# Kernel tuning notes

Measured on AMD Instinct MI355X. Metric: run time of the kernel, lower is better.

Reference implementation:

```python
import jax, jax.numpy as jnp
import numpy as np

DIM = 1024
B, S = 4, 2048

def setup_inputs() -> dict:
    key = jax.random.key(0)
    ks = jax.random.split(key, 4)
    x = jax.random.normal(ks[0], (B, S, DIM), dtype=jnp.float32)
    mask = jax.random.randint(ks[1], (B, S, S), 0, 2, dtype=jnp.int32)
    Wqkv = jax.random.normal(ks[2], (DIM, 3 * DIM), dtype=jnp.float32) / np.sqrt(DIM)
    bqkv = jnp.zeros((3 * DIM,), dtype=jnp.float32)
    Wout = jax.random.normal(ks[3], (DIM, DIM), dtype=jnp.float32) / np.sqrt(DIM)
    bout = jnp.zeros((DIM,), dtype=jnp.float32)
    return {"x": x, "mask": mask, "Wqkv": Wqkv, "bqkv": bqkv, "Wout": Wout, "bout": bout}

def reference(x, mask, Wqkv, bqkv, Wout, bout):
    dim = x.shape[-1]
    qkv = x @ Wqkv + bqkv                      # [B,S,3*dim]
    q, k, v = jnp.split(qkv, 3, axis=-1)       # each [B,S,dim]
    scores = jnp.einsum('bqd,bkd->bqk', q, k) / jnp.sqrt(jnp.float32(dim))
    # faithful to torch: masked positions set to 1e-10 (NOT -inf)
    scores = jnp.where(mask == 0, jnp.float32(1e-10), scores)
    attn = jax.nn.softmax(scores, axis=-1)     # dropout is identity in eval
    out = jnp.einsum('bqk,bkd->bqd', attn, v)  # [B,S,dim]
    return out @ Wout + bout
```

## Files before the change

kernel.cpp:

```cpp
#include <hip/hip_runtime.h>


typedef __attribute__((ext_vector_type(8))) short short8;
typedef __attribute__((ext_vector_type(4))) float f32x4;
typedef unsigned short u16;

#define SEQ 2048
#define NB 4

static __device__ __forceinline__ u16 f2bf(float f) {
    unsigned int u = __builtin_bit_cast(unsigned int, f);
    u += 0x7fffu + ((u >> 16) & 1u);
    return (u16)(u >> 16);
}
static __device__ __forceinline__ float bf2f(u16 h) {
    unsigned int u = ((unsigned int)h) << 16;
    return __builtin_bit_cast(float, u);
}

static __device__ __forceinline__ void gld16(const u16* l, const u16* g) {
    __builtin_amdgcn_global_load_lds(
        (__attribute__((address_space(1))) void*)(g),
        (__attribute__((address_space(3))) void*)(l),
        16, 0, 0);
}

__global__ __launch_bounds__(256) void cvt_bf16(const float* __restrict__ s,
                                                u16* __restrict__ d, long n) {
    long i = ((long)blockIdx.x * 256 + threadIdx.x) * 8;
    if (i >= n) return;
    f32x4 a = *(const f32x4*)(s + i);
    f32x4 b = *(const f32x4*)(s + i + 4);
    short8 o;
    o[0] = (short)f2bf(a.x); o[1] = (short)f2bf(a.y);
    o[2] = (short)f2bf(a.z); o[3] = (short)f2bf(a.w);
    o[4] = (short)f2bf(b.x); o[5] = (short)f2bf(b.y);
    o[6] = (short)f2bf(b.z); o[7] = (short)f2bf(b.w);
    *(short8*)(d + i) = o;
}

__global__ __launch_bounds__(256) void transpose_cvt(const float* __restrict__ in,
                                                     u16* __restrict__ out,
                                                     int R, int C) {
    __shared__ float t[32][33];
    const int c0 = blockIdx.x * 32;
    const int r0 = blockIdx.y * 32;
    const int x = threadIdx.x & 31;
    const int y = (threadIdx.x >> 5) * 4;
    #pragma unroll
    for (int i = 0; i < 4; i++)
        t[y + i][x] = in[(long)(r0 + y + i) * C + c0 + x];
    __syncthreads();
    #pragma unroll
    for (int i = 0; i < 4; i++)
        out[(long)(c0 + y + i) * R + r0 + x] = f2bf(t[x][y + i]);
}

__global__ __launch_bounds__(256) void transpose_v(const u16* __restrict__ qkv,
                                                   u16* __restrict__ vt) {
    __shared__ u16 t[32][33];
    const int b = blockIdx.z;
    const int s0 = blockIdx.y * 32;
    const int d0 = blockIdx.x * 32;
    const int x = threadIdx.x & 31;
    const int y = (threadIdx.x >> 5) * 4;
    const u16* src = qkv + (long)b * SEQ * 3072 + 2048;
    u16* dst = vt + (long)b * 1024 * SEQ;
    #pragma unroll
    for (int i = 0; i < 4; i++)
        t[y + i][x] = src[(long)(s0 + y + i) * 3072 + d0 + x];
    __syncthreads();
    #pragma unroll
    for (int i = 0; i < 4; i++)
        dst[(long)(d0 + y + i) * SEQ + s0 + x] = t[x][y + i];
}

template<int EPI>
__global__ __launch_bounds__(512) void gemm256(
    const u16* __restrict__ Ap, long lda, long aBatch,
    const u16* __restrict__ Bp, long ldb, long bBatch,
    void* __restrict__ Cp, long ldc, long cBatch,
    const float* __restrict__ bias, float scale, int K, int nbx)
{
    __shared__ __attribute__((aligned(16))) u16 lds[2][4][8192];

    const int T = K >> 6;
    const int tid = threadIdx.x;
    const int lane = tid & 63;
    const int wave = tid >> 6;
    const int wm = wave >> 2;
    const int wn = wave & 3;
    const int m16 = lane & 15;
    const int quad = lane >> 4;
    const int b = blockIdx.z;

    const int nwg = gridDim.x;
    int wg = blockIdx.x;
    if ((nwg & 7) == 0)
        wg = (wg & 7) * (nwg >> 3) + (wg >> 3);
    const int bx = wg % nbx;
    const int by = wg / nbx;
    const long gm0 = (long)by * 256;
    const long gn0 = (long)bx * 256;

    const u16* A = Ap + (long)b * aBatch;
    const u16* B = Bp + (long)b * bBatch;

    const int rl = lane >> 3;
    const int lsl = ((lane & 7) ^ rl) * 8;
    const long aR = gm0 + wave * 8 + rl;
    const long bR = gn0 + (wave >> 2) * 64 + (wave & 3) * 8 + rl;

#define STG_A(h, tt) do { \
    const int tc_ = ((tt) < T) ? (tt) : (tt) - 2; \
    const long kc_ = (long)(tc_ << 6); \
    const int sl_ = tc_ & 1; \
    gld16(&lds[sl_][h][wave * 512],       A + (aR + (h) * 64) * lda + kc_ + lsl); \
    gld16(&lds[sl_][h][(8 + wave) * 512], A + (aR + 128 + (h) * 64) * lda + kc_ + lsl); \
} while (0)
#define STG_B(h, tt) do { \
    const int tc_ = ((tt) < T) ? (tt) : (tt) - 2; \
    const long kc_ = (long)(tc_ << 6); \
    const int sl_ = tc_ & 1; \
    gld16(&lds[sl_][2 + (h)][wave * 512],       B + (bR + (h) * 32) * ldb + kc_ + lsl); \
    gld16(&lds[sl_][2 + (h)][(8 + wave) * 512], B + (bR + 128 + (h) * 32) * ldb + kc_ + lsl); \
} while (0)

    const int s0 = quad ^ (m16 & 7);
    const int aBase = (wm * 64 + m16) * 64;
    const int bBase = (wn * 32 + m16) * 64;
    const int aoff0 = aBase + s0 * 8, aoff1 = aBase + (s0 ^ 4) * 8;
    const int boff0 = bBase + s0 * 8, boff1 = bBase + (s0 ^ 4) * 8;

    short8 aF[4][2], b0F[2][2], b1F[2][2];
    f32x4 acc[8][4];
    #pragma unroll
    for (int mi = 0; mi < 8; mi++)
        #pragma unroll
        for (int ni = 0; ni < 4; ni++)
            acc[mi][ni] = (f32x4){0.f, 0.f, 0.f, 0.f};

#define LD_A(sl, h) do { \
    const u16* p_ = &lds[sl][h][0]; \
    _Pragma("unroll") \
    for (int mfl_ = 0; mfl_ < 4; ++mfl_) { \
        aF[mfl_][0] = *(const short8*)(p_ + aoff0 + mfl_ * 1024); \
        aF[mfl_][1] = *(const short8*)(p_ + aoff1 + mfl_ * 1024); \
    } \
} while (0)
#define LD_B(sl, h, BF) do { \
    const u16* p_ = &lds[sl][2 + (h)][0]; \
    _Pragma("unroll") \
    for (int nj_ = 0; nj_ < 2; ++nj_) { \
        BF[nj_][0] = *(const short8*)(p_ + boff0 + nj_ * 1024); \
        BF[nj_][1] = *(const short8*)(p_ + boff1 + nj_ * 1024); \
    } \
} while (0)
#define MFMAQ(mh, nh, BF) do { \
    _Pragma("unroll") \
    for (int mi_ = 0; mi_ < 4; ++mi_) \
    _Pragma("unroll") \
    for (int nj_ = 0; nj_ < 2; ++nj_) { \
        acc[(mh)*4+mi_][(nh)*2+nj_] = __builtin_amdgcn_mfma_f32_16x16x32_bf16( \
            aF[mi_][0], BF[nj_][0], acc[(mh)*4+mi_][(nh)*2+nj_], 0, 0, 0); \
        acc[(mh)*4+mi_][(nh)*2+nj_] = __builtin_amdgcn_mfma_f32_16x16x32_bf16( \
            aF[mi_][1], BF[nj_][1], acc[(mh)*4+mi_][(nh)*2+nj_], 0, 0, 0); \
    } \
} while (0)
#define BAR() asm volatile("s_barrier" ::: "memory")
#define VM8() asm volatile("s_waitcnt vmcnt(8)" ::: "memory")
#define SETP(p) __builtin_amdgcn_s_setprio(p)

    STG_A(0, 0); STG_B(0, 0); STG_B(1, 0); STG_A(1, 0);
    STG_A(0, 1); STG_B(0, 1); STG_B(1, 1); STG_A(1, 1);
    VM8();
    BAR();
    LD_B(0, 0, b0F);

    for (int t = 0; t < T; ++t) {
        const int buf = t & 1, nb = buf ^ 1;
        LD_A(buf, 0);
        SETP(1); MFMAQ(0, 0, b0F); SETP(0);
        BAR();
        LD_B(buf, 1, b1F);
        STG_A(0, t + 2);
        STG_B(0, t + 2);
        SETP(1); MFMAQ(0, 1, b1F); SETP(0);
        BAR();
        LD_A(buf, 1);
        STG_B(1, t + 2);
        SETP(1); MFMAQ(1, 0, b0F); SETP(0);
        BAR();
        STG_A(1, t + 2);
        VM8();
        BAR();
        LD_B(nb, 0, b0F);
        SETP(1); MFMAQ(1, 1, b1F); SETP(0);
    }

    const long row0 = gm0 + wm * 128 + quad * 4;
    if (EPI == 0 || EPI == 1) {
        u16* C = (u16*)Cp + (long)b * cBatch;
        #pragma unroll
        for (int ni = 0; ni < 4; ++ni) {
            const long col = gn0 + wn * 64 + (ni >> 1) * 32 + (ni & 1) * 16 + m16;
            const float bv = (EPI == 0 && bias) ? bias[col] : 0.f;
            #pragma unroll
            for (int mi = 0; mi < 8; ++mi) {
                const long rb = row0 + (mi >> 2) * 64 + (mi & 3) * 16;
                #pragma unroll
                for (int r = 0; r < 4; ++r) {
                    const float vv = (EPI == 1) ? acc[mi][ni][r] * scale
                                                : acc[mi][ni][r] + bv;
                    C[(rb + r) * ldc + col] = f2bf(vv);
                }
            }
        }
    } else {
        float* C = (float*)Cp + (long)b * cBatch;
        #pragma unroll
        for (int ni = 0; ni < 4; ++ni) {
            const long col = gn0 + wn * 64 + (ni >> 1) * 32 + (ni & 1) * 16 + m16;
            const float bv = bias ? bias[col] : 0.f;
            #pragma unroll
            for (int mi = 0; mi < 8; ++mi) {
                const long rb = row0 + (mi >> 2) * 64 + (mi & 3) * 16;
                #pragma unroll
                for (int r = 0; r < 4; ++r)
                    C[(rb + r) * ldc + col] = acc[mi][ni][r] + bv;
            }
        }
    }
#undef STG_A
#undef STG_B
#undef LD_A
#undef LD_B
#undef MFMAQ
#undef BAR
#undef VM8
#undef SETP
}

template<int EPI>
__global__ __launch_bounds__(256) void gemm128(
    const u16* __restrict__ Ap, long lda, long aBatch,
    const u16* __restrict__ Bp, long ldb, long bBatch,
    void* __restrict__ Cp, long ldc, long cBatch,
    const float* __restrict__ bias,
    float scale, int K)
{
    __shared__ __attribute__((aligned(16))) u16 As[128 * 64];
    __shared__ __attribute__((aligned(16))) u16 Bs[128 * 64];

    const int tid = threadIdx.x;
    const int lane = tid & 63;
    const int wave = tid >> 6;
    const int b = blockIdx.z;
    const long m0 = (long)blockIdx.y * 128;
    const long n0 = (long)blockIdx.x * 128;

    const u16* A = Ap + (long)b * aBatch;
    const u16* B = Bp + (long)b * bBatch;

    const int wm = (wave >> 1) * 64;
    const int wn = (wave & 1) * 64;
    const int m16 = lane & 15;
    const int quad = lane >> 4;

    const int srow = lane >> 3;
    const int skk = (lane & 7) * 8;

    f32x4 acc[4][4];
    #pragma unroll
    for (int mi = 0; mi < 4; mi++)
        #pragma unroll
        for (int ni = 0; ni < 4; ni++)
            acc[mi][ni] = (f32x4){0.f, 0.f, 0.f, 0.f};

    for (int k0 = 0; k0 < K; k0 += 64) {
        #pragma unroll
        for (int c = 0; c < 4; c++) {
            const int r = wave * 32 + c * 8 + srow;
            gld16(As + (wave * 4 + c) * 512, A + (m0 + r) * lda + k0 + skk);
            gld16(Bs + (wave * 4 + c) * 512, B + (n0 + r) * ldb + k0 + skk);
        }
        __syncthreads();

        #pragma unroll
        for (int ks = 0; ks < 2; ks++) {
            short8 af[4], bf[4];
            #pragma unroll
            for (int i = 0; i < 4; i++) {
                af[i] = *(const short8*)&As[(wm + i * 16 + m16) * 64 + ks * 32 + quad * 8];
                bf[i] = *(const short8*)&Bs[(wn + i * 16 + m16) * 64 + ks * 32 + quad * 8];
            }
            #pragma unroll
            for (int mi = 0; mi < 4; mi++)
                #pragma unroll
                for (int ni = 0; ni < 4; ni++)
                    acc[mi][ni] = __builtin_amdgcn_mfma_f32_16x16x32_bf16(
                        af[mi], bf[ni], acc[mi][ni], 0, 0, 0);
        }
        __syncthreads();
    }

    const long row_base = m0 + wm + quad * 4;
    if (EPI == 0) {
        u16* C = (u16*)Cp + (long)b * cBatch;
        #pragma unroll
        for (int ni = 0; ni < 4; ni++) {
            const long col = n0 + wn + ni * 16 + m16;
            const float bv = bias ? bias[col] : 0.f;
            #pragma unroll
            for (int mi = 0; mi < 4; mi++)
                #pragma unroll
                for (int r = 0; r < 4; r++)
                    C[(row_base + mi * 16 + r) * ldc + col] = f2bf(acc[mi][ni][r] + bv);
        }
    } else if (EPI == 1) {
        u16* C = (u16*)Cp + (long)b * cBatch;
        #pragma unroll
        for (int ni = 0; ni < 4; ni++) {
            const long col = n0 + wn + ni * 16 + m16;
            #pragma unroll
            for (int mi = 0; mi < 4; mi++)
                #pragma unroll
                for (int r = 0; r < 4; r++)
                    C[(row_base + mi * 16 + r) * ldc + col] = f2bf(acc[mi][ni][r] * scale);
        }
    } else {
        float* C = (float*)Cp + (long)b * cBatch;
        #pragma unroll
        for (int ni = 0; ni < 4; ni++) {
            const long col = n0 + wn + ni * 16 + m16;
            const float bv = bias ? bias[col] : 0.f;
            #pragma unroll
            for (int mi = 0; mi < 4; mi++)
                #pragma unroll
                for (int r = 0; r < 4; r++)
                    C[(row_base + mi * 16 + r) * ldc + col] = acc[mi][ni][r] + bv;
        }
    }
}

__global__ __launch_bounds__(256) void softmax2048(u16* __restrict__ S,
                                                   const int* __restrict__ mask) {
    const long row = blockIdx.x;
    u16* p = S + row * SEQ;
    const int* mrow = mask + row * SEQ;
    const int tid = threadIdx.x;

    short8 v = *(const short8*)(p + tid * 8);
    uint4 mw0 = *(const uint4*)(mrow + tid * 8);
    uint4 mw1 = *(const uint4*)(mrow + tid * 8 + 4);
    const unsigned int* mwv = (const unsigned int*)&mw0;

    float f[8];
    #pragma unroll
    for (int j = 0; j < 8; j++) {
        const unsigned int mv = (j < 4) ? mwv[j] : ((const unsigned int*)&mw1)[j - 4];
        f[j] = (mv == 0u) ? 1e-10f : bf2f((u16)v[j]);
    }

    float m = f[0];
    #pragma unroll
    for (int j = 1; j < 8; j++) m = fmaxf(m, f[j]);
    #pragma unroll
    for (int i = 1; i < 64; i <<= 1) m = fmaxf(m, __shfl_xor(m, i));

    __shared__ float redm[4], reds[4];
    if ((tid & 63) == 0) redm[tid >> 6] = m;
    __syncthreads();
    m = fmaxf(fmaxf(redm[0], redm[1]), fmaxf(redm[2], redm[3]));

    float e[8], s = 0.f;
    #pragma unroll
    for (int j = 0; j < 8; j++) { e[j] = __expf(f[j] - m); s += e[j]; }
    #pragma unroll
    for (int i = 1; i < 64; i <<= 1) s += __shfl_xor(s, i);
    if ((tid & 63) == 0) reds[tid >> 6] = s;
    __syncthreads();
    s = reds[0] + reds[1] + reds[2] + reds[3];

    const float inv = 1.f / s;
    short8 o;
    #pragma unroll
    for (int j = 0; j < 8; j++) o[j] = (short)f2bf(e[j] * inv);
    *(short8*)(p + tid * 8) = o;
}

extern "C" void kernel_launch(void* const* d_in, const int* in_sizes, int n_in,
                              void* d_out, int out_size, void* d_ws, size_t ws_size,
                              hipStream_t stream) {
    const float* x    = (const float*)d_in[0];
    const int*   mask = (const int*)d_in[1];
    const float* Wqkv = (const float*)d_in[2];
    const float* bqkv = (const float*)d_in[3];
    const float* Wout = (const float*)d_in[4];
    const float* bout = (const float*)d_in[5];
    float* out = (float*)d_out;

    char* ws = (char*)d_ws;
    u16* xh   = (u16*)(ws + 0);
    u16* wqt  = (u16*)(ws + 16777216);
    u16* sc   = (u16*)(ws + 0);
    u16* wot  = (u16*)(ws + 33554432);
    u16* qkv  = (u16*)(ws + 35651584);
    u16* attn = (u16*)(ws + 35651584);
    u16* vt   = (u16*)(ws + 85983232);

    cvt_bf16<<<4096, 256, 0, stream>>>(x, xh, 8388608);
    transpose_cvt<<<dim3(96, 32), 256, 0, stream>>>(Wqkv, wqt, 1024, 3072);
    transpose_cvt<<<dim3(32, 32), 256, 0, stream>>>(Wout, wot, 1024, 1024);

    gemm256<0><<<dim3(384, 1, 1), 512, 0, stream>>>(
        xh, 1024, 0, wqt, 1024, 0, qkv, 3072, 0, bqkv, 1.f, 1024, 12);

    transpose_v<<<dim3(32, 64, NB), 256, 0, stream>>>(qkv, vt);

    gemm256<1><<<dim3(64, 1, NB), 512, 0, stream>>>(
        qkv, 3072, (long)SEQ * 3072, qkv + 1024, 3072, (long)SEQ * 3072,
        sc, SEQ, (long)SEQ * SEQ, nullptr, 0.03125f, 1024, 8);

    softmax2048<<<dim3(NB * SEQ), 256, 0, stream>>>(sc, mask);

    gemm128<0><<<dim3(8, 16, NB), 256, 0, stream>>>(
        sc, SEQ, (long)SEQ * SEQ, vt, SEQ, (long)1024 * SEQ,
        attn, 1024, (long)SEQ * 1024, nullptr, 1.f, 2048);

    gemm128<2><<<dim3(8, 64, 1), 256, 0, stream>>>(
        attn, 1024, 0, wot, 1024, 0, out, 1024, 0, bout, 1.f, 1024);
}
```

Measured before the change: 236.0 us.

## Restructure 8-wave GEMM main loop into barrier-fenced MFMA phases with shifted staging

Reorders the software pipeline of the 256x256 GEMM main loop: each MFMA quarter is now wrapped in barriers, an LDS wait, and scheduling barriers. Global-to-LDS staging of one B half is delayed by one iteration, with vmcnt thresholds adjusted to match. The aim is a ping-pong style schedule where memory and MFMA phases alternate cleanly and the compiler cannot interleave them. It adds extra barriers per iteration and carries a risk of stalls or hazards if the shifted staging order and wait counts are off.

```diff
diff --git a/kernel.cpp b/kernel.cpp
--- a/kernel.cpp
+++ b/kernel.cpp
@@ -169,33 +169,39 @@
 } while (0)
 #define BAR() asm volatile("s_barrier" ::: "memory")
 #define VM8() asm volatile("s_waitcnt vmcnt(8)" ::: "memory")
+#define VM10() asm volatile("s_waitcnt vmcnt(10)" ::: "memory")
+#define LGKM8() asm volatile("s_waitcnt lgkmcnt(8)" ::: "memory")
+#define LGKM0() asm volatile("s_waitcnt lgkmcnt(0)" ::: "memory")
+#define SGB0() __builtin_amdgcn_sched_barrier(0)
 #define SETP(p) __builtin_amdgcn_s_setprio(p)
-
-    STG_A(0, 0); STG_B(0, 0); STG_B(1, 0); STG_A(1, 0);
-    STG_A(0, 1); STG_B(0, 1); STG_B(1, 1); STG_A(1, 1);
-    VM8();
+#define PHASE_MFMA(mh, nh, BF) do { \
+    BAR(); LGKM0(); SGB0(); \
+    SETP(1); MFMAQ(mh, nh, BF); SETP(0); \
+    SGB0(); BAR(); \
+} while (0)
+
+    STG_A(0, 0); STG_B(0, 0); STG_A(1, 0); STG_B(1, 0);
+    STG_A(0, 1); STG_B(0, 1); STG_A(1, 1);
+    VM10();
     BAR();
-    LD_B(0, 0, b0F);
 
     for (int t = 0; t < T; ++t) {
-        const int buf = t & 1, nb = buf ^ 1;
+        const int buf = t & 1;
         LD_A(buf, 0);
-        SETP(1); MFMAQ(0, 0, b0F); SETP(0);
-        BAR();
+        LD_B(buf, 0, b0F);
+        STG_B(1, t + 1);
+        LGKM8();
+        VM8();
+        PHASE_MFMA(0, 0, b0F);
         LD_B(buf, 1, b1F);
         STG_A(0, t + 2);
+        PHASE_MFMA(0, 1, b1F);
+        LD_A(buf, 1);
         STG_B(0, t + 2);
-        SETP(1); MFMAQ(0, 1, b1F); SETP(0);
-        BAR();
-        LD_A(buf, 1);
-        STG_B(1, t + 2);
-        SETP(1); MFMAQ(1, 0, b0F); SETP(0);
-        BAR();
+        PHASE_MFMA(1, 0, b0F);
         STG_A(1, t + 2);
-        VM8();
-        BAR();
-        LD_B(nb, 0, b0F);
-        SETP(1); MFMAQ(1, 1, b1F); SETP(0);
+        VM10();
+        PHASE_MFMA(1, 1, b1F);
     }
 
     const long row0 = gm0 + wm * 128 + quad * 4;
@@ -238,7 +244,12 @@
 #undef MFMAQ
 #undef BAR
 #undef VM8
+#undef VM10
+#undef LGKM8
+#undef LGKM0
+#undef SGB0
 #undef SETP
+#undef PHASE_MFMA
 }
 
 template<int EPI>
```

Measured after the change: 238.2 us. No clear change (+0.9%).

## Replace interleaved gemm256 pipeline with simple double-buffered tile loop

Applied to the files above, without the earlier changes.

Replaces the four-phase interleaved stage/compute schedule in the 256x256 GEMM with a plain double-buffer scheme. Each tile's loads are issued into the other LDS buffer, then all A/B fragments are computed, with a full __syncthreads between tiles. This drops the fine-grained barriers, the vmcnt waits and the MFMA priority hints. It also reorders the epilogue loops in both GEMM kernels so each thread writes along a row, with bias values hoisted. It risks less overlap between load and compute and higher register pressure, since all B fragments are held at once.

```diff
diff --git a/kernel.cpp b/kernel.cpp
--- a/kernel.cpp
+++ b/kernel.cpp
@@ -76,7 +76,7 @@
 }
 
 template<int EPI>
-__global__ __launch_bounds__(512) void gemm256(
+__global__ __launch_bounds__(512) void gemm256d(
     const u16* __restrict__ Ap, long lda, long aBatch,
     const u16* __restrict__ Bp, long ldb, long bBatch,
     void* __restrict__ Cp, long ldc, long cBatch,
@@ -111,19 +111,17 @@
     const long aR = gm0 + wave * 8 + rl;
     const long bR = gn0 + (wave >> 2) * 64 + (wave & 3) * 8 + rl;
 
-#define STG_A(h, tt) do { \
-    const int tc_ = ((tt) < T) ? (tt) : (tt) - 2; \
-    const long kc_ = (long)(tc_ << 6); \
-    const int sl_ = tc_ & 1; \
-    gld16(&lds[sl_][h][wave * 512],       A + (aR + (h) * 64) * lda + kc_ + lsl); \
-    gld16(&lds[sl_][h][(8 + wave) * 512], A + (aR + 128 + (h) * 64) * lda + kc_ + lsl); \
-} while (0)
-#define STG_B(h, tt) do { \
-    const int tc_ = ((tt) < T) ? (tt) : (tt) - 2; \
-    const long kc_ = (long)(tc_ << 6); \
-    const int sl_ = tc_ & 1; \
-    gld16(&lds[sl_][2 + (h)][wave * 512],       B + (bR + (h) * 32) * ldb + kc_ + lsl); \
-    gld16(&lds[sl_][2 + (h)][(8 + wave) * 512], B + (bR + 128 + (h) * 32) * ldb + kc_ + lsl); \
+#define STGD(sl, tt) do { \
+    const long kc_ = (long)(tt) << 6; \
+    u16* l_ = &lds[sl][0][0]; \
+    gld16(l_ + 0 * 8192 + wave * 512,       A + (aR)       * lda + kc_ + lsl); \
+    gld16(l_ + 0 * 8192 + (8 + wave) * 512, A + (aR + 128) * lda + kc_ + lsl); \
+    gld16(l_ + 1 * 8192 + wave * 512,       A + (aR + 64)  * lda + kc_ + lsl); \
+    gld16(l_ + 1 * 8192 + (8 + wave) * 512, A + (aR + 192) * lda + kc_ + lsl); \
+    gld16(l_ + 2 * 8192 + wave * 512,       B + (bR)       * ldb + kc_ + lsl); \
+    gld16(l_ + 2 * 8192 + (8 + wave) * 512, B + (bR + 128) * ldb + kc_ + lsl); \
+    gld16(l_ + 3 * 8192 + wave * 512,       B + (bR + 32)  * ldb + kc_ + lsl); \
+    gld16(l_ + 3 * 8192 + (8 + wave) * 512, B + (bR + 160) * ldb + kc_ + lsl); \
 } while (0)
 
     const int s0 = quad ^ (m16 & 7);
@@ -140,105 +138,102 @@
         for (int ni = 0; ni < 4; ni++)
             acc[mi][ni] = (f32x4){0.f, 0.f, 0.f, 0.f};
 
-#define LD_A(sl, h) do { \
-    const u16* p_ = &lds[sl][h][0]; \
+#define TILE_COMPUTE(sl) do { \
+    const u16* l = &lds[sl][0][0]; \
     _Pragma("unroll") \
-    for (int mfl_ = 0; mfl_ < 4; ++mfl_) { \
-        aF[mfl_][0] = *(const short8*)(p_ + aoff0 + mfl_ * 1024); \
-        aF[mfl_][1] = *(const short8*)(p_ + aoff1 + mfl_ * 1024); \
+    for (int mfl = 0; mfl < 4; ++mfl) { \
+        aF[mfl][0] = *(const short8*)(l + aoff0 + mfl * 1024); \
+        aF[mfl][1] = *(const short8*)(l + aoff1 + mfl * 1024); \
     } \
+    _Pragma("unroll") \
+    for (int nj = 0; nj < 2; ++nj) { \
+        b0F[nj][0] = *(const short8*)(l + 2 * 8192 + boff0 + nj * 1024); \
+        b0F[nj][1] = *(const short8*)(l + 2 * 8192 + boff1 + nj * 1024); \
+        b1F[nj][0] = *(const short8*)(l + 3 * 8192 + boff0 + nj * 1024); \
+        b1F[nj][1] = *(const short8*)(l + 3 * 8192 + boff1 + nj * 1024); \
+    } \
+    _Pragma("unroll") \
+    for (int mi = 0; mi < 4; ++mi) \
+        _Pragma("unroll") \
+        for (int nj = 0; nj < 4; ++nj) { \
+            const short8* bf = (nj < 2) ? &b0F[nj][0] : &b1F[nj - 2][0]; \
+            acc[mi][nj] = __builtin_amdgcn_mfma_f32_16x16x32_bf16( \
+                aF[mi][0], bf[0], acc[mi][nj], 0, 0, 0); \
+            acc[mi][nj] = __builtin_amdgcn_mfma_f32_16x16x32_bf16( \
+                aF[mi][1], bf[1], acc[mi][nj], 0, 0, 0); \
+        } \
+    _Pragma("unroll") \
+    for (int mfl = 0; mfl < 4; ++mfl) { \
+        aF[mfl][0] = *(const short8*)(l + 1 * 8192 + aoff0 + mfl * 1024); \
+        aF[mfl][1] = *(const short8*)(l + 1 * 8192 + aoff1 + mfl * 1024); \
+    } \
+    _Pragma("unroll") \
+    for (int mi = 0; mi < 4; ++mi) \
+        _Pragma("unroll") \
+        for (int nj = 0; nj < 4; ++nj) { \
+            const short8* bf = (nj < 2) ? &b0F[nj][0] : &b1F[nj - 2][0]; \
+            acc[4 + mi][nj] = __builtin_amdgcn_mfma_f32_16x16x32_bf16( \
+                aF[mi][0], bf[0], acc[4 + mi][nj], 0, 0, 0); \
+            acc[4 + mi][nj] = __builtin_amdgcn_mfma_f32_16x16x32_bf16( \
+                aF[mi][1], bf[1], acc[4 + mi][nj], 0, 0, 0); \
+        } \
 } while (0)
-#define LD_B(sl, h, BF) do { \
-    const u16* p_ = &lds[sl][2 + (h)][0]; \
-    _Pragma("unroll") \
-    for (int nj_ = 0; nj_ < 2; ++nj_) { \
-        BF[nj_][0] = *(const short8*)(p_ + boff0 + nj_ * 1024); \
-        BF[nj_][1] = *(const short8*)(p_ + boff1 + nj_ * 1024); \
-    } \
-} while (0)
-#define MFMAQ(mh, nh, BF) do { \
-    _Pragma("unroll") \
-    for (int mi_ = 0; mi_ < 4; ++mi_) \
-    _Pragma("unroll") \
-    for (int nj_ = 0; nj_ < 2; ++nj_) { \
-        acc[(mh)*4+mi_][(nh)*2+nj_] = __builtin_amdgcn_mfma_f32_16x16x32_bf16( \
-            aF[mi_][0], BF[nj_][0], acc[(mh)*4+mi_][(nh)*2+nj_], 0, 0, 0); \
-        acc[(mh)*4+mi_][(nh)*2+nj_] = __builtin_amdgcn_mfma_f32_16x16x32_bf16( \
-            aF[mi_][1], BF[nj_][1], acc[(mh)*4+mi_][(nh)*2+nj_], 0, 0, 0); \
-    } \
-} while (0)
-#define BAR() asm volatile("s_barrier" ::: "memory")
-#define VM8() asm volatile("s_waitcnt vmcnt(8)" ::: "memory")
-#define SETP(p) __builtin_amdgcn_s_setprio(p)
-
-    STG_A(0, 0); STG_B(0, 0); STG_B(1, 0); STG_A(1, 0);
-    STG_A(0, 1); STG_B(0, 1); STG_B(1, 1); STG_A(1, 1);
-    VM8();
-    BAR();
-    LD_B(0, 0, b0F);
-
-    for (int t = 0; t < T; ++t) {
-        const int buf = t & 1, nb = buf ^ 1;
-        LD_A(buf, 0);
-        SETP(1); MFMAQ(0, 0, b0F); SETP(0);
-        BAR();
-        LD_B(buf, 1, b1F);
-        STG_A(0, t + 2);
-        STG_B(0, t + 2);
-        SETP(1); MFMAQ(0, 1, b1F); SETP(0);
-        BAR();
-        LD_A(buf, 1);
-        STG_B(1, t + 2);
-        SETP(1); MFMAQ(1, 0, b0F); SETP(0);
-        BAR();
-        STG_A(1, t + 2);
-        VM8();
-        BAR();
-        LD_B(nb, 0, b0F);
-        SETP(1); MFMAQ(1, 1, b1F); SETP(0);
+
+    STGD(0, 0);
+    __syncthreads();
+
+    for (int t = 0; t < T; t += 2) {
+        if (t + 1 < T) STGD(1, t + 1);
+        TILE_COMPUTE(0);
+        __syncthreads();
+        if (t + 2 < T) STGD(0, t + 2);
+        TILE_COMPUTE(1);
+        __syncthreads();
     }
 
     const long row0 = gm0 + wm * 128 + quad * 4;
+    const long colbase = gn0 + wn * 64 + m16;
     if (EPI == 0 || EPI == 1) {
         u16* C = (u16*)Cp + (long)b * cBatch;
-        #pragma unroll
-        for (int ni = 0; ni < 4; ++ni) {
-            const long col = gn0 + wn * 64 + (ni >> 1) * 32 + (ni & 1) * 16 + m16;
-            const float bv = (EPI == 0 && bias) ? bias[col] : 0.f;
-            #pragma unroll
-            for (int mi = 0; mi < 8; ++mi) {
-                const long rb = row0 + (mi >> 2) * 64 + (mi & 3) * 16;
-                #pragma unroll
-                for (int r = 0; r < 4; ++r) {
+        float bv[4];
+        #pragma unroll
+        for (int ni = 0; ni < 4; ++ni)
+            bv[ni] = (EPI == 0 && bias)
+                   ? bias[colbase + (ni >> 1) * 32 + (ni & 1) * 16] : 0.f;
+        #pragma unroll
+        for (int mi = 0; mi < 8; ++mi) {
+            const long rb = row0 + (mi >> 2) * 64 + (mi & 3) * 16;
+            #pragma unroll
+            for (int r = 0; r < 4; ++r) {
+                u16* Crow = C + (rb + r) * ldc + colbase;
+                #pragma unroll
+                for (int ni = 0; ni < 4; ++ni) {
                     const float vv = (EPI == 1) ? acc[mi][ni][r] * scale
-                                                : acc[mi][ni][r] + bv;
-                    C[(rb + r) * ldc + col] = f2bf(vv);
+                                                : acc[mi][ni][r] + bv[ni];
+                    Crow[(ni >> 1) * 32 + (ni & 1) * 16] = f2bf(vv);
                 }
             }
         }
     } else {
         float* C = (float*)Cp + (long)b * cBatch;
-        #pragma unroll
-        for (int ni = 0; ni < 4; ++ni) {
-            const long col = gn0 + wn * 64 + (ni >> 1) * 32 + (ni & 1) * 16 + m16;
-            const float bv = bias ? bias[col] : 0.f;
-            #pragma unroll
-            for (int mi = 0; mi < 8; ++mi) {
-                const long rb = row0 + (mi >> 2) * 64 + (mi & 3) * 16;
-                #pragma unroll
-                for (int r = 0; r < 4; ++r)
-                    C[(rb + r) * ldc + col] = acc[mi][ni][r] + bv;
+        float bv[4];
+        #pragma unroll
+        for (int ni = 0; ni < 4; ++ni)
+            bv[ni] = bias ? bias[colbase + (ni >> 1) * 32 + (ni & 1) * 16] : 0.f;
+        #pragma unroll
+        for (int mi = 0; mi < 8; ++mi) {
+            const long rb = row0 + (mi >> 2) * 64 + (mi & 3) * 16;
+            #pragma unroll
+            for (int r = 0; r < 4; ++r) {
+                float* Crow = C + (rb + r) * ldc + colbase;
+                #pragma unroll
+                for (int ni = 0; ni < 4; ++ni)
+                    Crow[(ni >> 1) * 32 + (ni & 1) * 16] = acc[mi][ni][r] + bv[ni];
             }
         }
     }
-#undef STG_A
-#undef STG_B
-#undef LD_A
-#undef LD_B
-#undef MFMAQ
-#undef BAR
-#undef VM8
-#undef SETP
+#undef STGD
+#undef TILE_COMPUTE
 }
 
 template<int EPI>
@@ -305,41 +300,48 @@
     }
 
     const long row_base = m0 + wm + quad * 4;
+    const long colbase = n0 + wn + m16;
     if (EPI == 0) {
         u16* C = (u16*)Cp + (long)b * cBatch;
-        #pragma unroll
-        for (int ni = 0; ni < 4; ni++) {
-            const long col = n0 + wn + ni * 16 + m16;
-            const float bv = bias ? bias[col] : 0.f;
-            #pragma unroll
-            for (int mi = 0; mi < 4; mi++)
-                #pragma unroll
-                for (int r = 0; r < 4; r++)
-                    C[(row_base + mi * 16 + r) * ldc + col] = f2bf(acc[mi][ni][r] + bv);
-        }
+        float bv[4];
+        #pragma unroll
+        for (int ni = 0; ni < 4; ni++)
+            bv[ni] = bias ? bias[colbase + ni * 16] : 0.f;
+        #pragma unroll
+        for (int mi = 0; mi < 4; mi++)
+            #pragma unroll
+            for (int r = 0; r < 4; r++) {
+                u16* Crow = C + (row_base + mi * 16 + r) * ldc + colbase;
+                #pragma unroll
+                for (int ni = 0; ni < 4; ni++)
+                    Crow[ni * 16] = f2bf(acc[mi][ni][r] + bv[ni]);
+            }
     } else if (EPI == 1) {
         u16* C = (u16*)Cp + (long)b * cBatch;
         #pragma unroll
-        for (int ni = 0; ni < 4; ni++) {
-            const long col = n0 + wn + ni * 16 + m16;
-            #pragma unroll
-            for (int mi = 0; mi < 4; mi++)
-                #pragma unroll
-                for (int r = 0; r < 4; r++)
-                    C[(row_base + mi * 16 + r) * ldc + col] = f2bf(acc[mi][ni][r] * scale);
-        }
+        for (int mi = 0; mi < 4; mi++)
+            #pragma unroll
+            for (int r = 0; r < 4; r++) {
+                u16* Crow = C + (row_base + mi * 16 + r) * ldc + colbase;
+                #pragma unroll
+                for (int ni = 0; ni < 4; ni++)
+                    Crow[ni * 16] = f2bf(acc[mi][ni][r] * scale);
+            }
     } else {
         float* C = (float*)Cp + (long)b * cBatch;
-        #pragma unroll
-        for (int ni = 0; ni < 4; ni++) {
-            const long col = n0 + wn + ni * 16 + m16;
-            const float bv = bias ? bias[col] : 0.f;
-            #pragma unroll
-            for (int mi = 0; mi < 4; mi++)
-                #pragma unroll
-                for (int r = 0; r < 4; r++)
-                    C[(row_base + mi * 16 + r) * ldc + col] = acc[mi][ni][r] + bv;
-        }
+        float bv[4];
+        #pragma unroll
+        for (int ni = 0; ni < 4; ni++)
+            bv[ni] = bias ? bias[colbase + ni * 16] : 0.f;
+        #pragma unroll
+        for (int mi = 0; mi < 4; mi++)
+            #pragma unroll
+            for (int r = 0; r < 4; r++) {
+                float* Crow = C + (row_base + mi * 16 + r) * ldc + colbase;
+                #pragma unroll
+                for (int ni = 0; ni < 4; ni++)
+                    Crow[ni * 16] = acc[mi][ni][r] + bv[ni];
+            }
     }
 }
 
@@ -413,12 +415,12 @@
     transpose_cvt<<<dim3(96, 32), 256, 0, stream>>>(Wqkv, wqt, 1024, 3072);
     transpose_cvt<<<dim3(32, 32), 256, 0, stream>>>(Wout, wot, 1024, 1024);
 
-    gemm256<0><<<dim3(384, 1, 1), 512, 0, stream>>>(
+    gemm256d<0><<<dim3(384, 1, 1), 512, 0, stream>>>(
         xh, 1024, 0, wqt, 1024, 0, qkv, 3072, 0, bqkv, 1.f, 1024, 12);
 
     transpose_v<<<dim3(32, 64, NB), 256, 0, stream>>>(qkv, vt);
 
-    gemm256<1><<<dim3(64, 1, NB), 512, 0, stream>>>(
+    gemm256d<1><<<dim3(64, 1, NB), 512, 0, stream>>>(
         qkv, 3072, (long)SEQ * 3072, qkv + 1024, 3072, (long)SEQ * 3072,
         sc, SEQ, (long)SEQ * SEQ, nullptr, 0.03125f, 1024, 8);
 
```

New measurement: 221.4 us. 6.2% less time.
